# Optimization experiments

Measured on AMD Instinct MI355X. Metric: run time of the kernel, lower is better.

The kernel has to match this reference:

```python
import jax, jax.numpy as jnp
import numpy as np

# ---- fan-beam CT geometry (hard-coded in fidelity_module) ----
N = 256                      # image is N x N on [-20, 20]^2
A = 20                       # number of projection angles over [0, 2pi)
UDET = 624                   # detector pixels on [-60, 60]
S = 768                      # ray samples for line-integral quadrature
R_SRC = 59.0                 # source-to-origin radius
R_DET = 49.0                 # detector-to-origin radius
D_SD = R_SRC + R_DET         # source-to-detector distance
XMIN, XMAX = -20.0, 20.0
DX = (XMAX - XMIN) / N
UMIN, UMAX = -60.0, 60.0
DU = (UMAX - UMIN) / UDET
THETAS = ((np.arange(A) + 0.5) * 2.0 * np.pi / A).astype(np.float32)   # cell midpoints (odl.uniform_partition)
UCENT = (UMIN + (np.arange(UDET) + 0.5) * DU).astype(np.float32)       # detector cell midpoints
NFFT = 2048                  # FFT length for ramp filtering (>= 2*UDET)


def _bilinear(img, gx, gy):
    """img: [B,N,N] (axis0=x, axis1=y). gx, gy: fractional index coords, shape [...].
    Returns [B, ...] with zero outside the image."""
    i0 = jnp.floor(gx)
    j0 = jnp.floor(gy)
    fx = (gx - i0).astype(img.dtype)
    fy = (gy - j0).astype(img.dtype)
    i0 = i0.astype(jnp.int32)
    j0 = j0.astype(jnp.int32)

    def corner(ii, jj):
        valid = (ii >= 0) & (ii < N) & (jj >= 0) & (jj < N)
        v = img[:, jnp.clip(ii, 0, N - 1), jnp.clip(jj, 0, N - 1)]
        return jnp.where(valid[None], v, 0.0)

    return (corner(i0, j0) * (1 - fx) * (1 - fy)
            + corner(i0 + 1, j0) * fx * (1 - fy)
            + corner(i0, j0 + 1) * (1 - fx) * fy
            + corner(i0 + 1, j0 + 1) * fx * fy)


def forward_project(img):
    """Ray-driven fan-beam forward projection (Radon transform). img: [B,N,N] -> sino [B,A,UDET]."""
    cs = jnp.cos(jnp.asarray(THETAS))
    sn = jnp.sin(jnp.asarray(THETAS))
    src = R_SRC * jnp.stack([cs, sn], axis=-1)            # (A,2) source positions
    det_c = -R_DET * jnp.stack([cs, sn], axis=-1)         # (A,2) detector centers
    ddir = jnp.stack([-sn, cs], axis=-1)                  # (A,2) detector axis
    u = jnp.asarray(UCENT)
    p = det_c[:, None, :] + u[None, :, None] * ddir[:, None, :]   # (A,U,2) detector pixel positions
    ray = p - src[:, None, :]                             # (A,U,2)
    length = jnp.sqrt(jnp.sum(ray * ray, axis=-1))        # (A,U) ray length
    tt = (jnp.arange(S, dtype=jnp.float32) + 0.5) / S     # (S,) midpoint quadrature
    pts = src[:, None, None, :] + tt[None, None, :, None] * ray[:, :, None, :]  # (A,U,S,2)
    gx = (pts[..., 0] - XMIN) / DX - 0.5                  # fractional index along axis0 (x)
    gy = (pts[..., 1] - XMIN) / DX - 0.5                  # fractional index along axis1 (y)
    vals = _bilinear(img, gx, gy)                         # (B,A,U,S)
    return jnp.sum(vals, axis=-1) * (length / S)[None]    # (B,A,U)


def fbp(sino):
    """Filtered back-projection with Hann-windowed ramp filter (frequency_scaling=1).
    sino: [B,A,UDET] -> image [B,N,N]."""
    u = jnp.asarray(UCENT)
    # cosine pre-weighting for flat fan-beam detector
    g = sino * (D_SD / jnp.sqrt(D_SD * D_SD + u * u))[None, None, :]
    freqs = jnp.fft.rfftfreq(NFFT, d=DU).astype(jnp.float32)
    nyq = 1.0 / (2.0 * DU)
    ramp = jnp.abs(freqs)
    hann = 0.5 * (1.0 + jnp.cos(np.float32(np.pi) * freqs / nyq)) * (freqs <= nyq)
    filt = ramp * hann
    q = jnp.fft.irfft(jnp.fft.rfft(g, n=NFFT, axis=-1) * filt[None, None, :], n=NFFT, axis=-1)
    q = q[..., :UDET] * DU                                # (B,A,U) filtered sinogram

    cs = jnp.cos(jnp.asarray(THETAS))
    sn = jnp.sin(jnp.asarray(THETAS))
    xs = XMIN + (jnp.arange(N, dtype=jnp.float32) + 0.5) * DX
    X = xs[:, None]                                       # axis0 = x
    Y = xs[None, :]                                       # axis1 = y
    # distance from source plane to pixel along central ray: in [R_SRC-28, R_SRC+28], never ~0
    tdist = R_SRC - (X[None] * cs[:, None, None] + Y[None] * sn[:, None, None])   # (A,N,N)
    uu = D_SD * (-X[None] * sn[:, None, None] + Y[None] * cs[:, None, None]) / tdist  # detector coord of pixel
    k = (uu - UCENT[0]) / DU                              # fractional detector index (A,N,N)
    k0 = jnp.floor(k)
    fk = (k - k0).astype(sino.dtype)
    k0 = k0.astype(jnp.int32)
    aidx = jnp.arange(A)[:, None, None]

    def gather(kk):
        valid = (kk >= 0) & (kk < UDET)
        v = q[:, aidx, jnp.clip(kk, 0, UDET - 1)]         # (B,A,N,N)
        return jnp.where(valid[None], v, 0.0)

    val = gather(k0) * (1 - fk)[None] + gather(k0 + 1) * fk[None]
    w = (R_SRC / tdist) ** 2                              # fan-beam distance weighting
    dtheta = 2.0 * np.pi / A
    return 0.5 * np.float32(dtheta) * jnp.sum(w[None] * val, axis=1)  # (B,N,N)


def setup_inputs() -> dict:
    key = jax.random.key(0)
    k1, k2 = jax.random.split(key)
    input_data = jax.random.uniform(k1, (4, N, N), dtype=jnp.float32)
    proj = jax.random.normal(k2, (4, A, UDET), dtype=jnp.float32)
    return {"input_data": input_data, "proj": proj}


def reference(input_data, proj):
    # fidelity_module.forward: x_error = FBP(proj - Radon(input_data))
    p_tmp = forward_project(input_data)
    y_error = proj - p_tmp
    return fbp(y_error)
```

## Files before the change

kernel.cpp:

```cpp
#include <hip/hip_runtime.h>
#include <math.h>

#define NN 256
#define AA 20
#define UD 624
#define SS 768
#define NAU (AA*UD)
#define PI_D 3.14159265358979323846

__global__ void k_transpose(const float* __restrict__ img, float4* __restrict__ imgT) {
    int idx = blockIdx.x * 256 + threadIdx.x;
    float4 v;
    v.x = img[idx];
    v.y = img[65536 + idx];
    v.z = img[131072 + idx];
    v.w = img[196608 + idx];
    imgT[idx] = v;
}

__global__ void k_hh(float* __restrict__ hh) {
    __shared__ double red[256];
    const int n = blockIdx.x;
    const int tid = threadIdx.x;
    double acc = 0.0;
    for (int k = 1 + tid; k < 1024; k += 256) {
        float a1 = 1.0f + cosf((float)PI_D * (float)k * (1.0f/1024.0f));
        int m = (k * n) & 2047;
        float c2 = cosf((float)PI_D * (float)m * (1.0f/1024.0f));
        acc += (double)((float)k * a1 * c2);
    }
    red[tid] = acc;
    __syncthreads();
    for (int s = 128; s > 0; s >>= 1) {
        if (tid < s) red[tid] += red[tid + s];
        __syncthreads();
    }
    if (tid == 0) hh[n] = (float)(red[0] * (1.0 / (2048.0 * 2048.0)));
}

__global__ __launch_bounds__(64) void k_forward(const float4* __restrict__ imgT,
                                                const float* __restrict__ proj,
                                                float* __restrict__ g) {
    const int blk = blockIdx.x;
    const int a = blk / UD;
    const int u = blk - a * UD;
    const int tid = threadIdx.x;

    const float theta = (float)(((double)a + 0.5) * (2.0 * PI_D / (double)AA));
    float sn, cs;
    sincosf(theta, &sn, &cs);
    const float uc = (float)(-60.0 + ((double)u + 0.5) * (120.0 / 624.0));

    const float sx = 59.0f * cs, sy = 59.0f * sn;
    const float px = -49.0f * cs - uc * sn;
    const float py = -49.0f * sn + uc * cs;
    const float rx = px - sx, ry = py - sy;
    const float length = sqrtf(rx * rx + ry * ry);

    float ax = 0.f, ay = 0.f, az = 0.f, aw = 0.f;

    for (int s = tid; s < SS; s += 64) {
        float t = ((float)s + 0.5f) * (1.0f / 768.0f);
        float x = sx + t * rx;
        float y = sy + t * ry;
        float gx = (x + 20.0f) * 6.4f - 0.5f;
        float gy = (y + 20.0f) * 6.4f - 0.5f;
        float fgx = floorf(gx), fgy = floorf(gy);
        float fx = gx - fgx, fy = gy - fgy;
        int i0 = (int)fgx, j0 = (int)fgy;
        int i1 = i0 + 1, j1 = j0 + 1;
        float wx0 = (i0 >= 0 && i0 < NN) ? (1.0f - fx) : 0.0f;
        float wx1 = (i1 >= 0 && i1 < NN) ? fx : 0.0f;
        float wy0 = (j0 >= 0 && j0 < NN) ? (1.0f - fy) : 0.0f;
        float wy1 = (j1 >= 0 && j1 < NN) ? fy : 0.0f;
        int ic0 = min(max(i0, 0), NN - 1), ic1 = min(max(i1, 0), NN - 1);
        int jc0 = min(max(j0, 0), NN - 1), jc1 = min(max(j1, 0), NN - 1);
        float4 c00 = imgT[ic0 * NN + jc0];
        float4 c10 = imgT[ic1 * NN + jc0];
        float4 c01 = imgT[ic0 * NN + jc1];
        float4 c11 = imgT[ic1 * NN + jc1];
        float w00 = wx0 * wy0, w10 = wx1 * wy0, w01 = wx0 * wy1, w11 = wx1 * wy1;
        ax += w00 * c00.x + w10 * c10.x + w01 * c01.x + w11 * c11.x;
        ay += w00 * c00.y + w10 * c10.y + w01 * c01.y + w11 * c11.y;
        az += w00 * c00.z + w10 * c10.z + w01 * c01.z + w11 * c11.z;
        aw += w00 * c00.w + w10 * c10.w + w01 * c01.w + w11 * c11.w;
    }

    for (int off = 32; off > 0; off >>= 1) {
        ax += __shfl_down(ax, off);
        ay += __shfl_down(ay, off);
        az += __shfl_down(az, off);
        aw += __shfl_down(aw, off);
    }

    if (tid == 0) {
        const float scale = length * (1.0f / 768.0f);
        const float wdet = 108.0f / sqrtf(108.0f * 108.0f + uc * uc);
        g[0 * NAU + blk] = (proj[0 * NAU + blk] - ax * scale) * wdet;
        g[1 * NAU + blk] = (proj[1 * NAU + blk] - ay * scale) * wdet;
        g[2 * NAU + blk] = (proj[2 * NAU + blk] - az * scale) * wdet;
        g[3 * NAU + blk] = (proj[3 * NAU + blk] - aw * scale) * wdet;
    }
}

__global__ __launch_bounds__(640) void k_conv(const float* __restrict__ g,
                                              const float* __restrict__ hh,
                                              float* __restrict__ q) {
    __shared__ float sg[UD];
    __shared__ float sh[UD];
    const int row = blockIdx.x;
    const int tid = threadIdx.x;
    if (tid < UD) {
        sg[tid] = g[row * UD + tid];
        sh[tid] = hh[tid];
    }
    __syncthreads();
    if (tid < UD) {
        float acc = 0.0f;
        for (int i = 0; i < UD; ++i) {
            int d = tid - i;
            d = d < 0 ? -d : d;
            acc += sg[i] * sh[d];
        }
        q[row * UD + tid] = acc;
    }
}

__global__ __launch_bounds__(256) void k_bp(const float* __restrict__ q,
                                            float* __restrict__ out) {
    __shared__ float scs[AA], ssn[AA];
    const int tid = threadIdx.x;
    if (tid < AA) {
        float th = (float)(((double)tid + 0.5) * (2.0 * PI_D / (double)AA));
        float s, c;
        sincosf(th, &s, &c);
        scs[tid] = c;
        ssn[tid] = s;
    }
    __syncthreads();

    const int p = blockIdx.x * 256 + tid;
    const int b = p >> 16;
    const int rem = p & 65535;
    const int i = rem >> 8;
    const int j = rem & 255;

    const float X = -20.0f + ((float)i + 0.5f) * 0.15625f;
    const float Y = -20.0f + ((float)j + 0.5f) * 0.15625f;

    const float uc0 = (float)(-60.0 + 0.5 * (120.0 / 624.0));
    const float duf = (float)(120.0 / 624.0);

    const float* qb = q + b * AA * UD;
    float acc = 0.0f;
    for (int a = 0; a < AA; ++a) {
        float cs = scs[a], sn = ssn[a];
        float t = 59.0f - (X * cs + Y * sn);
        float uu = 108.0f * (Y * cs - X * sn) / t;
        float k = (uu - uc0) / duf;
        float fk0 = floorf(k);
        float fk = k - fk0;
        int ik = (int)fk0;
        const float* qr = qb + a * UD;
        float v0 = ((unsigned)ik < (unsigned)UD) ? qr[ik] : 0.0f;
        float v1 = ((unsigned)(ik + 1) < (unsigned)UD) ? qr[ik + 1] : 0.0f;
        float val = v0 * (1.0f - fk) + v1 * fk;
        float w = 59.0f / t;
        acc += w * w * val;
    }
    out[p] = (0.5f * (float)(2.0 * PI_D / (double)AA)) * acc;
}

extern "C" void kernel_launch(void* const* d_in, const int* in_sizes, int n_in,
                              void* d_out, int out_size, void* d_ws, size_t ws_size,
                              hipStream_t stream) {
    const float* img  = (const float*)d_in[0];
    const float* proj = (const float*)d_in[1];
    float* out = (float*)d_out;

    char* ws = (char*)d_ws;
    float4* imgT = (float4*)ws;
    float*  g    = (float*)(ws + (1 << 20));
    float*  q    = (float*)(ws + (1 << 20) + 199680);
    float*  hh   = (float*)(ws + (1 << 20) + 2 * 199680);

    k_transpose<<<256, 256, 0, stream>>>(img, imgT);
    k_hh<<<UD, 256, 0, stream>>>(hh);
    k_forward<<<NAU, 64, 0, stream>>>(imgT, proj, g);
    k_conv<<<AA * 4, 640, 0, stream>>>(g, hh, q);
    k_bp<<<1024, 256, 0, stream>>>(q, out);
}
```

Baseline: 119.3 us.

## Merge prep kernels, add transposed image copy, retile forward and convolution kernels

The transpose and filter-kernel setup are fused into a single prep launch that also writes a second, transposed copy of the image. Each forward ray samples whichever copy keeps consecutive samples contiguous along its dominant direction, which should improve cache locality of the bilinear gathers. The forward kernel now packs four rays per 256-thread block and steps sample coordinates incrementally. The convolution is split into five tiles per row with a zero-padded shared buffer and wave-uniform loop bounds, reading hh from global memory, and the backprojection angle loop is unrolled. The cost is an extra 1 MB image copy plus added branching and register use.

Measured after the change: 114.3 us. 4.2% less time.

```diff
diff --git a/kernel.cpp b/kernel.cpp
--- a/kernel.cpp
+++ b/kernel.cpp
@@ -8,43 +8,59 @@
 #define NAU (AA*UD)
 #define PI_D 3.14159265358979323846
 
-__global__ void k_transpose(const float* __restrict__ img, float4* __restrict__ imgT) {
-    int idx = blockIdx.x * 256 + threadIdx.x;
-    float4 v;
-    v.x = img[idx];
-    v.y = img[65536 + idx];
-    v.z = img[131072 + idx];
-    v.w = img[196608 + idx];
-    imgT[idx] = v;
-}
-
-__global__ void k_hh(float* __restrict__ hh) {
+__global__ __launch_bounds__(256) void k_prep(const float* __restrict__ img,
+                                              float4* __restrict__ pixA,
+                                              float4* __restrict__ pixB,
+                                              float* __restrict__ hh) {
     __shared__ double red[256];
-    const int n = blockIdx.x;
+    const int blk = blockIdx.x;
     const int tid = threadIdx.x;
-    double acc = 0.0;
-    for (int k = 1 + tid; k < 1024; k += 256) {
-        float a1 = 1.0f + cosf((float)PI_D * (float)k * (1.0f/1024.0f));
-        int m = (k * n) & 2047;
-        float c2 = cosf((float)PI_D * (float)m * (1.0f/1024.0f));
-        acc += (double)((float)k * a1 * c2);
-    }
-    red[tid] = acc;
-    __syncthreads();
-    for (int s = 128; s > 0; s >>= 1) {
-        if (tid < s) red[tid] += red[tid + s];
+    if (blk < 256) {
+        int idx = blk * 256 + tid;
+        float4 v;
+        v.x = img[idx];
+        v.y = img[65536 + idx];
+        v.z = img[131072 + idx];
+        v.w = img[196608 + idx];
+        pixA[idx] = v;
+    } else if (blk < 512) {
+        int oidx = (blk - 256) * 256 + tid;
+        int j = oidx >> 8, i = oidx & 255;
+        int idx = i * 256 + j;
+        float4 v;
+        v.x = img[idx];
+        v.y = img[65536 + idx];
+        v.z = img[131072 + idx];
+        v.w = img[196608 + idx];
+        pixB[oidx] = v;
+    } else {
+        const int n = blk - 512;
+        double acc = 0.0;
+        for (int k = 1 + tid; k < 1024; k += 256) {
+            float a1 = 1.0f + cosf((float)PI_D * (float)k * (1.0f/1024.0f));
+            int m = (k * n) & 2047;
+            float c2 = cosf((float)PI_D * (float)m * (1.0f/1024.0f));
+            acc += (double)((float)k * a1 * c2);
+        }
+        red[tid] = acc;
         __syncthreads();
-    }
-    if (tid == 0) hh[n] = (float)(red[0] * (1.0 / (2048.0 * 2048.0)));
-}
-
-__global__ __launch_bounds__(64) void k_forward(const float4* __restrict__ imgT,
-                                                const float* __restrict__ proj,
-                                                float* __restrict__ g) {
-    const int blk = blockIdx.x;
-    const int a = blk / UD;
-    const int u = blk - a * UD;
-    const int tid = threadIdx.x;
+        for (int s = 128; s > 0; s >>= 1) {
+            if (tid < s) red[tid] += red[tid + s];
+            __syncthreads();
+        }
+        if (tid == 0) hh[n] = (float)(red[0] * (1.0 / (2048.0 * 2048.0)));
+    }
+}
+
+__global__ __launch_bounds__(256) void k_forward(const float4* __restrict__ pixA,
+                                                 const float4* __restrict__ pixB,
+                                                 const float* __restrict__ proj,
+                                                 float* __restrict__ g) {
+    const int wid = threadIdx.x >> 6;
+    const int lane = threadIdx.x & 63;
+    const int ray = blockIdx.x * 4 + wid;
+    const int a = ray / UD;
+    const int u = ray - a * UD;
 
     const float theta = (float)(((double)a + 0.5) * (2.0 * PI_D / (double)AA));
     float sn, cs;
@@ -52,34 +68,42 @@
     const float uc = (float)(-60.0 + ((double)u + 0.5) * (120.0 / 624.0));
 
     const float sx = 59.0f * cs, sy = 59.0f * sn;
-    const float px = -49.0f * cs - uc * sn;
-    const float py = -49.0f * sn + uc * cs;
-    const float rx = px - sx, ry = py - sy;
+    const float rx = -108.0f * cs - uc * sn;
+    const float ry = -108.0f * sn + uc * cs;
     const float length = sqrtf(rx * rx + ry * ry);
 
+    const float stepx = rx * (6.4f / 768.0f);
+    const float basex = (sx + rx * (0.5f / 768.0f) + 20.0f) * 6.4f - 0.5f;
+    const float stepy = ry * (6.4f / 768.0f);
+    const float basey = (sy + ry * (0.5f / 768.0f) + 20.0f) * 6.4f - 0.5f;
+
+    const bool useB = fabsf(stepx) > fabsf(stepy);
+    const float4* __restrict__ im = useB ? pixB : pixA;
+    const float bi = useB ? basex : basey;
+    const float si = useB ? stepx : stepy;
+    const float bo = useB ? basey : basex;
+    const float so = useB ? stepy : stepx;
+
     float ax = 0.f, ay = 0.f, az = 0.f, aw = 0.f;
 
-    for (int s = tid; s < SS; s += 64) {
-        float t = ((float)s + 0.5f) * (1.0f / 768.0f);
-        float x = sx + t * rx;
-        float y = sy + t * ry;
-        float gx = (x + 20.0f) * 6.4f - 0.5f;
-        float gy = (y + 20.0f) * 6.4f - 0.5f;
-        float fgx = floorf(gx), fgy = floorf(gy);
-        float fx = gx - fgx, fy = gy - fgy;
-        int i0 = (int)fgx, j0 = (int)fgy;
-        int i1 = i0 + 1, j1 = j0 + 1;
-        float wx0 = (i0 >= 0 && i0 < NN) ? (1.0f - fx) : 0.0f;
-        float wx1 = (i1 >= 0 && i1 < NN) ? fx : 0.0f;
-        float wy0 = (j0 >= 0 && j0 < NN) ? (1.0f - fy) : 0.0f;
-        float wy1 = (j1 >= 0 && j1 < NN) ? fy : 0.0f;
+    for (int s = lane; s < SS; s += 64) {
+        float gi = fmaf((float)s, si, bi);
+        float go = fmaf((float)s, so, bo);
+        float fgi = floorf(gi), fgo = floorf(go);
+        float fi = gi - fgi, fo = go - fgo;
+        int i0 = (int)fgi, o0 = (int)fgo;
+        int i1 = i0 + 1, o1 = o0 + 1;
+        float wi0 = (i0 >= 0 && i0 < NN) ? (1.0f - fi) : 0.0f;
+        float wi1 = (i1 >= 0 && i1 < NN) ? fi : 0.0f;
+        float wo0 = (o0 >= 0 && o0 < NN) ? (1.0f - fo) : 0.0f;
+        float wo1 = (o1 >= 0 && o1 < NN) ? fo : 0.0f;
         int ic0 = min(max(i0, 0), NN - 1), ic1 = min(max(i1, 0), NN - 1);
-        int jc0 = min(max(j0, 0), NN - 1), jc1 = min(max(j1, 0), NN - 1);
-        float4 c00 = imgT[ic0 * NN + jc0];
-        float4 c10 = imgT[ic1 * NN + jc0];
-        float4 c01 = imgT[ic0 * NN + jc1];
-        float4 c11 = imgT[ic1 * NN + jc1];
-        float w00 = wx0 * wy0, w10 = wx1 * wy0, w01 = wx0 * wy1, w11 = wx1 * wy1;
+        int oc0 = min(max(o0, 0), NN - 1), oc1 = min(max(o1, 0), NN - 1);
+        const float4 c00 = im[oc0 * NN + ic0];
+        const float4 c10 = im[oc0 * NN + ic1];
+        const float4 c01 = im[oc1 * NN + ic0];
+        const float4 c11 = im[oc1 * NN + ic1];
+        float w00 = wi0 * wo0, w10 = wi1 * wo0, w01 = wi0 * wo1, w11 = wi1 * wo1;
         ax += w00 * c00.x + w10 * c10.x + w01 * c01.x + w11 * c11.x;
         ay += w00 * c00.y + w10 * c10.y + w01 * c01.y + w11 * c11.y;
         az += w00 * c00.z + w10 * c10.z + w01 * c01.z + w11 * c11.z;
@@ -93,37 +117,43 @@
         aw += __shfl_down(aw, off);
     }
 
-    if (tid == 0) {
+    if (lane == 0) {
         const float scale = length * (1.0f / 768.0f);
         const float wdet = 108.0f / sqrtf(108.0f * 108.0f + uc * uc);
-        g[0 * NAU + blk] = (proj[0 * NAU + blk] - ax * scale) * wdet;
-        g[1 * NAU + blk] = (proj[1 * NAU + blk] - ay * scale) * wdet;
-        g[2 * NAU + blk] = (proj[2 * NAU + blk] - az * scale) * wdet;
-        g[3 * NAU + blk] = (proj[3 * NAU + blk] - aw * scale) * wdet;
-    }
-}
-
-__global__ __launch_bounds__(640) void k_conv(const float* __restrict__ g,
+        g[0 * NAU + ray] = (proj[0 * NAU + ray] - ax * scale) * wdet;
+        g[1 * NAU + ray] = (proj[1 * NAU + ray] - ay * scale) * wdet;
+        g[2 * NAU + ray] = (proj[2 * NAU + ray] - az * scale) * wdet;
+        g[3 * NAU + ray] = (proj[3 * NAU + ray] - aw * scale) * wdet;
+    }
+}
+
+__global__ __launch_bounds__(128) void k_conv(const float* __restrict__ g,
                                               const float* __restrict__ hh,
                                               float* __restrict__ q) {
-    __shared__ float sg[UD];
-    __shared__ float sh[UD];
-    const int row = blockIdx.x;
+    __shared__ float sgp[752];
+    const int row = blockIdx.x / 5;
+    const int tile = blockIdx.x % 5;
     const int tid = threadIdx.x;
-    if (tid < UD) {
-        sg[tid] = g[row * UD + tid];
-        sh[tid] = hh[tid];
+
+    for (int k = tid; k < 752; k += 128) {
+        sgp[k] = (k >= 64 && k < 64 + UD) ? g[row * UD + (k - 64)] : 0.0f;
     }
     __syncthreads();
-    if (tid < UD) {
-        float acc = 0.0f;
-        for (int i = 0; i < UD; ++i) {
-            int d = tid - i;
-            d = d < 0 ? -d : d;
-            acc += sg[i] * sh[d];
-        }
-        q[row * UD + tid] = acc;
-    }
+
+    const int j = tile * 128 + tid;
+    const int jc = min(j, UD - 1);
+    int wbase = tile * 128 + (tid & 64);
+    wbase = __builtin_amdgcn_readfirstlane(wbase);
+    const int tmax1 = min(wbase + 63, UD - 1);
+    const int tmax2 = UD - 1 - wbase;
+
+    float acc = 0.0f;
+    for (int t = 0; t <= tmax1; ++t)
+        acc += hh[t] * sgp[64 + jc - t];
+    for (int t = 1; t <= tmax2; ++t)
+        acc += hh[t] * sgp[64 + jc + t];
+
+    if (j < UD) q[row * UD + j] = acc;
 }
 
 __global__ __launch_bounds__(256) void k_bp(const float* __restrict__ q,
@@ -151,8 +181,9 @@
     const float uc0 = (float)(-60.0 + 0.5 * (120.0 / 624.0));
     const float duf = (float)(120.0 / 624.0);
 
-    const float* qb = q + b * AA * UD;
+    const float* __restrict__ qb = q + b * AA * UD;
     float acc = 0.0f;
+#pragma unroll
     for (int a = 0; a < AA; ++a) {
         float cs = scs[a], sn = ssn[a];
         float t = 59.0f - (X * cs + Y * sn);
@@ -179,14 +210,14 @@
     float* out = (float*)d_out;
 
     char* ws = (char*)d_ws;
-    float4* imgT = (float4*)ws;
-    float*  g    = (float*)(ws + (1 << 20));
-    float*  q    = (float*)(ws + (1 << 20) + 199680);
-    float*  hh   = (float*)(ws + (1 << 20) + 2 * 199680);
-
-    k_transpose<<<256, 256, 0, stream>>>(img, imgT);
-    k_hh<<<UD, 256, 0, stream>>>(hh);
-    k_forward<<<NAU, 64, 0, stream>>>(imgT, proj, g);
-    k_conv<<<AA * 4, 640, 0, stream>>>(g, hh, q);
+    float4* pixA = (float4*)ws;
+    float4* pixB = (float4*)(ws + (1 << 20));
+    float*  g    = (float*)(ws + (2 << 20));
+    float*  q    = (float*)(ws + (2 << 20) + 199680);
+    float*  hh   = (float*)(ws + (2 << 20) + 2 * 199680);
+
+    k_prep<<<1136, 256, 0, stream>>>(img, pixA, pixB, hh);
+    k_forward<<<NAU / 4, 256, 0, stream>>>(pixA, pixB, proj, g);
+    k_conv<<<80 * 5, 128, 0, stream>>>(g, hh, q);
     k_bp<<<1024, 256, 0, stream>>>(q, out);
 }
```
